# Performance work log

Measured on AMD Instinct MI355X. Metric: run time of the kernel, lower is better.

The kernel has to match this reference:

```python
import jax, jax.numpy as jnp
import numpy as np

B, N, C = 16, 4096, 512
PW, PH = 64, 64  # N = PW * PH
POOL = 2         # attention_pool_scale
D_SCALE = 1.0 / float(np.sqrt(C))


def setup_inputs() -> dict:
    key = jax.random.key(0)
    ks = jax.random.split(key, 4)
    w_std = 1.0 / float(np.sqrt(C))
    return {
        "x": jax.random.normal(ks[0], (B, N, C), dtype=jnp.float32),
        "Wq": jax.random.normal(ks[1], (C, C), dtype=jnp.float32) * w_std,
        "bq": jnp.zeros((C,), dtype=jnp.float32),
        "Wk": jax.random.normal(ks[2], (C, C), dtype=jnp.float32) * w_std,
        "bk": jnp.zeros((C,), dtype=jnp.float32),
        "Wv": jax.random.normal(ks[3], (C, C), dtype=jnp.float32) * w_std,
        "bv": jnp.zeros((C,), dtype=jnp.float32),
    }


def _to_spatial(t):
    # [B, N, C] -> [B, C, PW, PH]
    return t.transpose(0, 2, 1).reshape(t.shape[0], C, PW, PH)


def reference(x, Wq, bq, Wk, bk, Wv, bv):
    # Linear (torch convention y = x @ W^T + b) + sigmoid activation
    def proj(W, b):
        return jax.nn.sigmoid(jnp.einsum('bnc,dc->bnd', x, W) + b)

    Q = _to_spatial(proj(Wq, bq))  # [B, C, PW, PH]
    K = _to_spatial(proj(Wk, bk))
    V = _to_spatial(proj(Wv, bv))

    # avg_pool2d with kernel (POOL, 1): pool over PW axis
    q = Q.reshape(B, C, PW // POOL, POOL, PH).mean(axis=3)  # [B, C, PW/2, PH]
    k = K.reshape(B, C, PW // POOL, POOL, PH).mean(axis=3)

    # Qk = softmax(scale * Q @ k^T): [B, C, PW, PW/2]
    Qk = jax.nn.softmax(D_SCALE * jnp.einsum('bcik,bcjk->bcij', Q, k), axis=-1)
    # Kq = softmax(scale * q @ K^T): [B, C, PW/2, PW]
    Kq = jax.nn.softmax(D_SCALE * jnp.einsum('bcik,bcjk->bcij', q, K), axis=-1)
    # Kqv = Kq @ V: [B, C, PW/2, PH]
    Kqv = jnp.einsum('bcij,bcjk->bcik', Kq, V)
    # out = Qk @ Kqv: [B, C, PW, PH]
    out = jnp.einsum('bcij,bcjk->bcik', Qk, Kqv)

    # spatial -> sequence: [B, C, PW*PH] -> [B, N, C]
    return out.reshape(B, C, N).transpose(0, 2, 1)
```

## Files before the change

kernel.cpp:

```cpp
#include <hip/hip_runtime.h>
#include <hip/hip_bf16.h>
#include <string.h>

typedef __hip_bfloat16  bf16;
typedef __hip_bfloat162 bf162;
typedef __attribute__((ext_vector_type(8))) short short8;
typedef __attribute__((ext_vector_type(4))) float f32x4;

#define NB 16
#define NN 4096
#define NC 512
#define SCALE 0.044194173824159216f

#define GLL16(gp, lp) __builtin_amdgcn_global_load_lds( \
    (__attribute__((address_space(1))) void*)(gp),      \
    (__attribute__((address_space(3))) void*)(lp), 16, 0, 0)

__global__ __launch_bounds__(256) void cast_x_kernel(
    const float* __restrict__ x, bf16* __restrict__ xb)
{
    size_t i = ((size_t)blockIdx.x * 256 + threadIdx.x) * 8;
    float4 a = *(const float4*)(x + i);
    float4 b = *(const float4*)(x + i + 4);
    bf16 t[8];
    t[0] = __float2bfloat16(a.x); t[1] = __float2bfloat16(a.y);
    t[2] = __float2bfloat16(a.z); t[3] = __float2bfloat16(a.w);
    t[4] = __float2bfloat16(b.x); t[5] = __float2bfloat16(b.y);
    t[6] = __float2bfloat16(b.z); t[7] = __float2bfloat16(b.w);
    uint4 r; memcpy(&r, t, 16);
    *(uint4*)(xb + i) = r;
}

__global__ __launch_bounds__(256) void cast_w_kernel(
    const float* __restrict__ Wq, const float* __restrict__ Wk,
    const float* __restrict__ Wv, bf16* __restrict__ Wb)
{
    const float* W = (blockIdx.y == 0) ? Wq : (blockIdx.y == 1) ? Wk : Wv;
    size_t i = ((size_t)blockIdx.x * 256 + threadIdx.x) * 8;
    float4 a = *(const float4*)(W + i);
    float4 b = *(const float4*)(W + i + 4);
    bf16 t[8];
    t[0] = __float2bfloat16(a.x); t[1] = __float2bfloat16(a.y);
    t[2] = __float2bfloat16(a.z); t[3] = __float2bfloat16(a.w);
    t[4] = __float2bfloat16(b.x); t[5] = __float2bfloat16(b.y);
    t[6] = __float2bfloat16(b.z); t[7] = __float2bfloat16(b.w);
    uint4 r; memcpy(&r, t, 16);
    *(uint4*)(Wb + (size_t)blockIdx.y * (NC * NC) + i) = r;
}

__global__ __launch_bounds__(256) void proj_mfma(
    const bf16* __restrict__ xb, const bf16* __restrict__ Wb,
    const float* __restrict__ bq, const float* __restrict__ bk,
    const float* __restrict__ bv,
    bf16* __restrict__ Qs, bf16* __restrict__ Ks, bf16* __restrict__ Vs)
{
    __shared__ __align__(16) char smem[32768];
    short* As = (short*)smem;
    short* Bs = (short*)(smem + 16384);
    float* st = (float*)smem;

    const int tid = threadIdx.x;
    const int w   = tid >> 6;
    const int l   = tid & 63;
    const int q   = l >> 4;
    const int mrow= l & 15;
    const int wr  = w >> 1;
    const int wc  = w & 1;

    const int bx = blockIdx.x;
    const int m  = bx >> 2;
    const int d0 = (bx & 3) * 128;
    const int r0 = blockIdx.y * 128;
    const int b  = r0 >> 12;
    const int n0 = r0 & 4095;

    const bf16*  W    = Wb + (size_t)m * (NC * NC);
    const float* bias = (m == 0) ? bq : (m == 1) ? bk : bv;
    bf16*        Out  = (m == 0) ? Qs : (m == 1) ? Ks : Vs;

    f32x4 acc[4][4];
    const f32x4 z = {0.f, 0.f, 0.f, 0.f};
    #pragma unroll
    for (int i = 0; i < 4; ++i)
        #pragma unroll
        for (int j = 0; j < 4; ++j) acc[i][j] = z;

    const int srow = tid >> 3;
    const int scol = (tid & 7) * 8;

    for (int k0 = 0; k0 < NC; k0 += 64) {
        #pragma unroll
        for (int c = 0; c < 4; ++c) {
            int row = srow + 32 * c;
            GLL16(xb + (size_t)(r0 + row) * NC + k0 + scol, &As[row * 64 + scol]);
        }
        #pragma unroll
        for (int c = 0; c < 4; ++c) {
            int row = srow + 32 * c;
            GLL16(W + (size_t)(d0 + row) * NC + k0 + scol, &Bs[row * 64 + scol]);
        }
        __syncthreads();

        #pragma unroll
        for (int ks = 0; ks < 2; ++ks) {
            short8 af[4], bfr[4];
            #pragma unroll
            for (int ti = 0; ti < 4; ++ti)
                af[ti] = *(const short8*)&As[(64 * wr + 16 * ti + mrow) * 64 + q * 8 + 32 * ks];
            #pragma unroll
            for (int tj = 0; tj < 4; ++tj)
                bfr[tj] = *(const short8*)&Bs[(64 * wc + 16 * tj + mrow) * 64 + q * 8 + 32 * ks];
            #pragma unroll
            for (int ti = 0; ti < 4; ++ti)
                #pragma unroll
                for (int tj = 0; tj < 4; ++tj)
                    acc[ti][tj] = __builtin_amdgcn_mfma_f32_16x16x32_bf16(
                        af[ti], bfr[tj], acc[ti][tj], 0, 0, 0);
        }
        __syncthreads();
    }

    float bb[4];
    #pragma unroll
    for (int tj = 0; tj < 4; ++tj) bb[tj] = bias[d0 + 64 * wc + 16 * tj + mrow];

    #pragma unroll
    for (int dc = 0; dc < 4; ++dc) {
        if (wc == (dc >> 1)) {
            #pragma unroll
            for (int tjh = 0; tjh < 2; ++tjh) {
                int tj = 2 * (dc & 1) + tjh;
                #pragma unroll
                for (int ti = 0; ti < 4; ++ti)
                    #pragma unroll
                    for (int g = 0; g < 4; ++g) {
                        float v  = acc[ti][tj][g] + bb[tj];
                        float sg = 1.0f / (1.0f + __expf(-v));
                        int nl = 64 * wr + 16 * ti + 4 * q + g;
                        int dl = 16 * tjh + mrow;
                        st[nl * 33 + dl] = sg;
                    }
            }
        }
        __syncthreads();
        #pragma unroll
        for (int i = 0; i < 8; ++i) {
            int p     = tid + 256 * i;
            int dl    = p >> 6;
            int npair = tid & 63;
            bf162 v2;
            v2.x = __float2bfloat16(st[(2 * npair    ) * 33 + dl]);
            v2.y = __float2bfloat16(st[(2 * npair + 1) * 33 + dl]);
            size_t d = d0 + 32 * dc + dl;
            ((bf162*)(Out + ((size_t)b * NC + d) * NN + n0))[npair] = v2;
        }
        __syncthreads();
    }
}

__global__ __launch_bounds__(256) void attn_mfma(
    const bf16* __restrict__ Qs, const bf16* __restrict__ Ks,
    const bf16* __restrict__ Vs, bf16* __restrict__ Os)
{
    __shared__ __align__(16) char smem[24064];
    bf16* VT  = (bf16*)smem;
    bf16* S1b = (bf16*)(smem + 9216);
    bf16* S2b = (bf16*)(smem + 9216 + 5120);
    bf16* KVT = (bf16*)(smem + 9216 + 5120 + 4608);

    const int tid = threadIdx.x;
    const int w   = tid >> 6;
    const int l   = tid & 63;
    const int m   = l & 15;
    const int q   = l >> 4;
    const size_t base = (size_t)blockIdx.x * NN;

    {
        const uint4* src = (const uint4*)(Vs + base);
        #pragma unroll
        for (int v = 0; v < 2; ++v) {
            int e = tid + 256 * v;
            uint4 r = src[e];
            bf16 tmp[8]; memcpy(tmp, &r, 16);
            int pw  = e >> 3;
            int ph0 = (e & 7) * 8;
            #pragma unroll
            for (int t = 0; t < 8; ++t)
                VT[(ph0 + t) * 72 + pw] = tmp[t];
        }
    }

    f32x4 tacc[4];
    {
        const f32x4 z = {0.f, 0.f, 0.f, 0.f};
        short8 aQ[2];
        #pragma unroll
        for (int ks = 0; ks < 2; ++ks)
            aQ[ks] = *(const short8*)(Qs + base + (16 * w + m) * 64 + q * 8 + 32 * ks);
        #pragma unroll
        for (int tj = 0; tj < 4; ++tj) {
            tacc[tj] = z;
            #pragma unroll
            for (int ks = 0; ks < 2; ++ks) {
                short8 bK = *(const short8*)(Ks + base + (16 * tj + m) * 64 + q * 8 + 32 * ks);
                tacc[tj] = __builtin_amdgcn_mfma_f32_16x16x32_bf16(aQ[ks], bK, tacc[tj], 0, 0, 0);
            }
        }
    }

    {
        float p[4][4], e[4][4], mx[4], s[4];
        #pragma unroll
        for (int r = 0; r < 4; ++r) mx[r] = -1e30f;
        #pragma unroll
        for (int t = 0; t < 4; ++t)
            #pragma unroll
            for (int r = 0; r < 4; ++r) {
                float v  = tacc[t][r];
                float pv = (v + __shfl_xor(v, 1)) * (0.5f * SCALE);
                p[t][r] = pv;
                mx[r]   = fmaxf(mx[r], pv);
            }
        #pragma unroll
        for (int r = 0; r < 4; ++r) {
            #pragma unroll
            for (int d = 1; d < 16; d <<= 1)
                mx[r] = fmaxf(mx[r], __shfl_xor(mx[r], d));
            s[r] = 0.f;
        }
        #pragma unroll
        for (int t = 0; t < 4; ++t)
            #pragma unroll
            for (int r = 0; r < 4; ++r) {
                e[t][r] = __expf(p[t][r] - mx[r]);
                s[r] += e[t][r];
            }
        #pragma unroll
        for (int r = 0; r < 4; ++r) {
            #pragma unroll
            for (int d = 1; d < 16; d <<= 1)
                s[r] += __shfl_xor(s[r], d);
            s[r] = 2.0f / s[r];
        }
        if (!(l & 1)) {
            int jc = m >> 1;
            #pragma unroll
            for (int t = 0; t < 4; ++t)
                #pragma unroll
                for (int r = 0; r < 4; ++r)
                    S1b[(16 * w + q * 4 + r) * 40 + t * 8 + jc] =
                        __float2bfloat16(e[t][r] * s[r]);
        }
    }

    {
        float p2[4][2], e2[4][2], mx[2], s[2];
        #pragma unroll
        for (int h = 0; h < 2; ++h) mx[h] = -1e30f;
        #pragma unroll
        for (int t = 0; t < 4; ++t)
            #pragma unroll
            for (int h = 0; h < 2; ++h) {
                float pv = (tacc[t][2 * h] + tacc[t][2 * h + 1]) * (0.5f * SCALE);
                p2[t][h] = pv;
                mx[h]    = fmaxf(mx[h], pv);
            }
        #pragma unroll
        for (int h = 0; h < 2; ++h) {
            #pragma unroll
            for (int d = 1; d < 16; d <<= 1)
                mx[h] = fmaxf(mx[h], __shfl_xor(mx[h], d));
            s[h] = 0.f;
        }
        #pragma unroll
        for (int t = 0; t < 4; ++t)
            #pragma unroll
            for (int h = 0; h < 2; ++h) {
                e2[t][h] = __expf(p2[t][h] - mx[h]);
                s[h] += e2[t][h];
            }
        #pragma unroll
        for (int h = 0; h < 2; ++h) {
            #pragma unroll
            for (int d = 1; d < 16; d <<= 1)
                s[h] += __shfl_xor(s[h], d);
            s[h] = 1.0f / s[h];
        }
        #pragma unroll
        for (int t = 0; t < 4; ++t)
            #pragma unroll
            for (int h = 0; h < 2; ++h)
                S2b[(8 * w + q * 2 + h) * 72 + t * 16 + m] =
                    __float2bfloat16(e2[t][h] * s[h]);
    }
    __syncthreads();

    {
        short8 aV[2];
        #pragma unroll
        for (int ks = 0; ks < 2; ++ks)
            aV[ks] = *(const short8*)&VT[(16 * w + m) * 72 + q * 8 + 32 * ks];
        #pragma unroll
        for (int tn = 0; tn < 2; ++tn) {
            f32x4 kacc = {0.f, 0.f, 0.f, 0.f};
            #pragma unroll
            for (int ks = 0; ks < 2; ++ks) {
                short8 bS = *(const short8*)&S2b[(16 * tn + m) * 72 + q * 8 + 32 * ks];
                kacc = __builtin_amdgcn_mfma_f32_16x16x32_bf16(aV[ks], bS, kacc, 0, 0, 0);
            }
            #pragma unroll
            for (int r = 0; r < 4; ++r)
                KVT[(16 * w + q * 4 + r) * 40 + 16 * tn + m] = __float2bfloat16(kacc[r]);
        }
    }
    __syncthreads();

    f32x4 oacc[4];
    {
        short8 aS = *(const short8*)&S1b[(16 * w + m) * 40 + q * 8];
        #pragma unroll
        for (int tn = 0; tn < 4; ++tn) {
            short8 bKV = *(const short8*)&KVT[(16 * tn + m) * 40 + q * 8];
            f32x4 z = {0.f, 0.f, 0.f, 0.f};
            oacc[tn] = __builtin_amdgcn_mfma_f32_16x16x32_bf16(aS, bKV, z, 0, 0, 0);
        }
    }

    {
        bf16* OutS = VT;
        #pragma unroll
        for (int tn = 0; tn < 4; ++tn)
            #pragma unroll
            for (int r = 0; r < 4; ++r)
                OutS[(16 * w + q * 4 + r) * 72 + 16 * tn + m] = __float2bfloat16(oacc[tn][r]);
        __syncthreads();
        uint* Og = (uint*)(Os + base);
        #pragma unroll
        for (int v = 0; v < 8; ++v) {
            int e  = tid + 256 * v;
            int i  = e >> 5;
            int pp = e & 31;
            Og[e] = *(uint*)&OutS[i * 72 + 2 * pp];
        }
    }
}

__global__ __launch_bounds__(256) void unspat_kernel(
    const bf16* __restrict__ Os, float* __restrict__ out)
{
    __shared__ float t[32][65];
    const int b  = blockIdx.z;
    const int c0 = blockIdx.y * 32;
    const int n0 = blockIdx.x * 64;
    const int tx = threadIdx.x & 31;
    const int ty = threadIdx.x >> 5;
    const bf162* src = (const bf162*)(Os + ((size_t)b * NC + c0) * NN + n0);
    #pragma unroll
    for (int r = 0; r < 4; ++r) {
        int cc = ty + r * 8;
        float2 f = __bfloat1622float2(src[(size_t)cc * (NN/2) + tx]);
        t[cc][2*tx] = f.x; t[cc][2*tx+1] = f.y;
    }
    __syncthreads();
    float* dst = out + ((size_t)b * NN + n0) * NC + c0;
    #pragma unroll
    for (int r = 0; r < 8; ++r) {
        int nn = ty + r * 8;
        dst[(size_t)nn * NC + tx] = t[tx][nn];
    }
}

extern "C" void kernel_launch(void* const* d_in, const int* in_sizes, int n_in,
                              void* d_out, int out_size, void* d_ws, size_t ws_size,
                              hipStream_t stream)
{
    const float* x  = (const float*)d_in[0];
    const float* Wq = (const float*)d_in[1];
    const float* bq = (const float*)d_in[2];
    const float* Wk = (const float*)d_in[3];
    const float* bk = (const float*)d_in[4];
    const float* Wv = (const float*)d_in[5];
    const float* bv = (const float*)d_in[6];
    float* out = (float*)d_out;

    const size_t S = (size_t)NB * NC * NN;
    bf16* Qb = (bf16*)d_ws;
    bf16* Kb = Qb + S;
    bf16* Vb = Kb + S;
    bf16* xb = (bf16*)d_out;
    bf16* Wb = ((bf16*)d_out) + S;

    cast_x_kernel<<<dim3((NB * NN * NC) / (256 * 8)), 256, 0, stream>>>(x, xb);
    cast_w_kernel<<<dim3((NC * NC) / (256 * 8), 3), 256, 0, stream>>>(Wq, Wk, Wv, Wb);
    proj_mfma<<<dim3(12, (NB * NN) / 128), 256, 0, stream>>>(
        xb, Wb, bq, bk, bv, Qb, Kb, Vb);
    attn_mfma<<<dim3(NB * NC), 256, 0, stream>>>(Qb, Kb, Vb, Qb);
    unspat_kernel<<<dim3(NN / 64, NC / 32, NB), 256, 0, stream>>>(Qb, out);
}
```

Before: 554.1 us.

## Swizzle projection LDS tiles, vectorize epilogue stores, shuffle-transpose V

The projection GEMM now fetches global data in an XOR-swizzled column order so that its LDS fragment reads avoid bank conflicts. The epilogue now writes each bf16 sigmoid result to a padded shared tile in a single pass and then emits 16-byte coalesced global stores. This replaces the four-round fp32 staging that needed two barriers per round. In the attention kernel, the V transpose into LDS now uses an 8x8 wavefront shuffle butterfly with vector LDS writes instead of scalar scattered 2-byte stores, at the cost of extra shuffle instructions.

```diff
diff --git a/kernel.cpp b/kernel.cpp
--- a/kernel.cpp
+++ b/kernel.cpp
@@ -54,10 +54,10 @@
     const float* __restrict__ bv,
     bf16* __restrict__ Qs, bf16* __restrict__ Ks, bf16* __restrict__ Vs)
 {
-    __shared__ __align__(16) char smem[32768];
+    __shared__ __align__(16) char smem[36864];
     short* As = (short*)smem;
     short* Bs = (short*)(smem + 16384);
-    float* st = (float*)smem;
+    bf16*  OutS = (bf16*)smem;
 
     const int tid = threadIdx.x;
     const int w   = tid >> 6;
@@ -87,17 +87,19 @@
 
     const int srow = tid >> 3;
     const int scol = (tid & 7) * 8;
+    const int sxor = ((tid ^ (tid >> 3)) & 7) * 8;
+    const int axor = (mrow & 7) * 8;
 
     for (int k0 = 0; k0 < NC; k0 += 64) {
         #pragma unroll
         for (int c = 0; c < 4; ++c) {
             int row = srow + 32 * c;
-            GLL16(xb + (size_t)(r0 + row) * NC + k0 + scol, &As[row * 64 + scol]);
+            GLL16(xb + (size_t)(r0 + row) * NC + k0 + sxor, &As[row * 64 + scol]);
         }
         #pragma unroll
         for (int c = 0; c < 4; ++c) {
             int row = srow + 32 * c;
-            GLL16(W + (size_t)(d0 + row) * NC + k0 + scol, &Bs[row * 64 + scol]);
+            GLL16(W + (size_t)(d0 + row) * NC + k0 + sxor, &Bs[row * 64 + scol]);
         }
         __syncthreads();
 
@@ -106,10 +108,12 @@
             short8 af[4], bfr[4];
             #pragma unroll
             for (int ti = 0; ti < 4; ++ti)
-                af[ti] = *(const short8*)&As[(64 * wr + 16 * ti + mrow) * 64 + q * 8 + 32 * ks];
+                af[ti] = *(const short8*)&As[(64 * wr + 16 * ti + mrow) * 64 +
+                                             ((q * 8 + 32 * ks) ^ axor)];
             #pragma unroll
             for (int tj = 0; tj < 4; ++tj)
-                bfr[tj] = *(const short8*)&Bs[(64 * wc + 16 * tj + mrow) * 64 + q * 8 + 32 * ks];
+                bfr[tj] = *(const short8*)&Bs[(64 * wc + 16 * tj + mrow) * 64 +
+                                              ((q * 8 + 32 * ks) ^ axor)];
             #pragma unroll
             for (int ti = 0; ti < 4; ++ti)
                 #pragma unroll
@@ -125,36 +129,28 @@
     for (int tj = 0; tj < 4; ++tj) bb[tj] = bias[d0 + 64 * wc + 16 * tj + mrow];
 
     #pragma unroll
-    for (int dc = 0; dc < 4; ++dc) {
-        if (wc == (dc >> 1)) {
-            #pragma unroll
-            for (int tjh = 0; tjh < 2; ++tjh) {
-                int tj = 2 * (dc & 1) + tjh;
-                #pragma unroll
-                for (int ti = 0; ti < 4; ++ti)
-                    #pragma unroll
-                    for (int g = 0; g < 4; ++g) {
-                        float v  = acc[ti][tj][g] + bb[tj];
-                        float sg = 1.0f / (1.0f + __expf(-v));
-                        int nl = 64 * wr + 16 * ti + 4 * q + g;
-                        int dl = 16 * tjh + mrow;
-                        st[nl * 33 + dl] = sg;
-                    }
-            }
-        }
-        __syncthreads();
-        #pragma unroll
-        for (int i = 0; i < 8; ++i) {
-            int p     = tid + 256 * i;
-            int dl    = p >> 6;
-            int npair = tid & 63;
-            bf162 v2;
-            v2.x = __float2bfloat16(st[(2 * npair    ) * 33 + dl]);
-            v2.y = __float2bfloat16(st[(2 * npair + 1) * 33 + dl]);
-            size_t d = d0 + 32 * dc + dl;
-            ((bf162*)(Out + ((size_t)b * NC + d) * NN + n0))[npair] = v2;
-        }
-        __syncthreads();
+    for (int ti = 0; ti < 4; ++ti)
+        #pragma unroll
+        for (int tj = 0; tj < 4; ++tj) {
+            int d = 64 * wc + 16 * tj + mrow;
+            bf16 t4[4];
+            #pragma unroll
+            for (int g = 0; g < 4; ++g) {
+                float v = acc[ti][tj][g] + bb[tj];
+                t4[g] = __float2bfloat16(1.0f / (1.0f + __expf(-v)));
+            }
+            uint2 pk; memcpy(&pk, t4, 8);
+            *(uint2*)&OutS[d * 144 + 64 * wr + 16 * ti + 4 * q] = pk;
+        }
+    __syncthreads();
+
+    #pragma unroll
+    for (int v = 0; v < 8; ++v) {
+        int e  = tid + 256 * v;
+        int d  = e >> 4;
+        int ch = e & 15;
+        uint4 r = *(const uint4*)&OutS[d * 144 + ch * 8];
+        *(uint4*)(Out + ((size_t)b * NC + d0 + d) * NN + n0 + ch * 8) = r;
     }
 }
 
@@ -176,17 +172,28 @@
     const size_t base = (size_t)blockIdx.x * NN;
 
     {
-        const uint4* src = (const uint4*)(Vs + base);
+        const int g = l >> 3;
         #pragma unroll
         for (int v = 0; v < 2; ++v) {
-            int e = tid + 256 * v;
-            uint4 r = src[e];
-            bf16 tmp[8]; memcpy(tmp, &r, 16);
-            int pw  = e >> 3;
-            int ph0 = (e & 7) * 8;
-            #pragma unroll
-            for (int t = 0; t < 8; ++t)
-                VT[(ph0 + t) * 72 + pw] = tmp[t];
+            int pw  = 8 * w + g + 32 * v;
+            int ph0 = (l & 7) * 8;
+            uint4 r4 = *(const uint4*)(Vs + base + pw * 64 + ph0);
+            ushort r[8]; memcpy(r, &r4, 16);
+            #pragma unroll
+            for (int mm = 1; mm < 8; mm <<= 1) {
+                const bool hi = (g & mm) != 0;
+                #pragma unroll
+                for (int j0 = 0; j0 < 8; ++j0) {
+                    if (!(j0 & mm)) {
+                        const int j1 = j0 | mm;
+                        int t = hi ? (int)r[j0] : (int)r[j1];
+                        t = __shfl_xor(t, mm << 3, 64);
+                        if (hi) r[j0] = (ushort)t; else r[j1] = (ushort)t;
+                    }
+                }
+            }
+            uint4 wv; memcpy(&wv, r, 16);
+            *(uint4*)&VT[(ph0 + g) * 72 + 8 * w + 32 * v] = wv;
         }
     }
 
```

Result: faster. 522.3 us (-5.7%).
